# Kernel tuning notes

Hardware: AMD Instinct MI355X
Metric: run time of the kernel (lower is better)

Reference implementation:

```python
import jax, jax.numpy as jnp
from jax import lax
import numpy as np

B, T, F, H, O = 4096, 2048, 8, 32, 8


def setup_inputs() -> dict:
    key = jax.random.key(0)
    k = jax.random.split(key, 7)
    s = 1.0 / np.sqrt(H).astype(np.float32)  # torch RNN/Linear init bound
    x = jax.random.normal(k[0], (B, T, F), dtype=jnp.float32)
    W_ih = jax.random.uniform(k[1], (H, F), minval=-s, maxval=s, dtype=jnp.float32)
    W_hh = jax.random.uniform(k[2], (H, H), minval=-s, maxval=s, dtype=jnp.float32)
    b_ih = jax.random.uniform(k[3], (H,), minval=-s, maxval=s, dtype=jnp.float32)
    b_hh = jax.random.uniform(k[4], (H,), minval=-s, maxval=s, dtype=jnp.float32)
    W_out = jax.random.uniform(k[5], (O, H), minval=-s, maxval=s, dtype=jnp.float32)
    b_out = jax.random.uniform(k[6], (O,), minval=-s, maxval=s, dtype=jnp.float32)
    return {"x": x, "W_ih": W_ih, "W_hh": W_hh, "b_ih": b_ih, "b_hh": b_hh,
            "W_out": W_out, "b_out": b_out}


def reference(x, W_ih, W_hh, b_ih, b_hh, W_out, b_out):
    # Precompute input projection for all timesteps: [B, T, H]
    xp = jnp.einsum('btf,hf->bth', x, W_ih) + b_ih + b_hh
    h0 = jnp.zeros((x.shape[0], W_hh.shape[0]), dtype=x.dtype)

    def step(h, xt):  # xt: [B, H]
        h = jnp.tanh(xt + h @ W_hh.T)
        return h, None

    h_final, _ = lax.scan(step, h0, jnp.swapaxes(xp, 0, 1))  # scan over T
    # torch returns out(h) with h of shape [num_layers=1, B, H]
    y = h_final @ W_out.T + b_out  # [B, O]
    return y[None]  # [1, B, O]
```

## Files before the change

kernel.cpp:

```cpp
#include <hip/hip_runtime.h>


typedef float v2f __attribute__((ext_vector_type(2)));
typedef _Float16 h2v __attribute__((ext_vector_type(2)));

static constexpr int T_STEPS = 2048;
static constexpr int FDIM    = 8;
static constexpr int HDIM    = 32;
static constexpr int ODIM    = 8;
static constexpr int ROWS_PER_BLOCK = 8;
static constexpr int GROUP   = 4;
static constexpr int NGROUP  = T_STEPS / GROUP;
static constexpr int LSTR    = 40;

__device__ __forceinline__ float fdot2(h2v a, h2v b, float c) {
    return __builtin_amdgcn_fdot2(a, b, c, false);
}
__device__ __forceinline__ h2v bch(unsigned u) {
    return __builtin_bit_cast(h2v, u);
}

__global__ __launch_bounds__(256, 2) void rnn_scan_kernel(
    const float* __restrict__ x,
    const float* __restrict__ W_ih,
    const float* __restrict__ W_hh,
    const float* __restrict__ b_ih,
    const float* __restrict__ b_hh,
    const float* __restrict__ W_out,
    const float* __restrict__ b_out,
    float* __restrict__ out)
{
    const float K = 2.8853900817779268f;
    const int tid  = threadIdx.x;
    const int lane = tid & 63;
    const int wave = tid >> 6;
    const int g    = lane & 15;
    const int c    = (lane >> 4) & 1;
    const int sub  = lane >> 5;
    const int r    = wave * 2 + sub;
    const long long b = (long long)blockIdx.x * ROWS_PER_BLOCK + r;
    const int d0 = 2 * g, d1 = 2 * g + 1;

    __shared__ _Float16 hsh[ROWS_PER_BLOCK][LSTR];

    h2v wA[8], wB[8];
    const float* whr0 = W_hh + d0 * HDIM + 16 * c;
    const float* whr1 = W_hh + d1 * HDIM + 16 * c;
#pragma unroll
    for (int j = 0; j < 8; ++j) {
        h2v wa; wa[0] = (_Float16)(whr0[2 * j] * K); wa[1] = (_Float16)(whr0[2 * j + 1] * K);
        wA[j] = wa;
        h2v wb; wb[0] = (_Float16)(whr1[2 * j] * K); wb[1] = (_Float16)(whr1[2 * j + 1] * K);
        wB[j] = wb;
    }
    v2f wiv[4];
#pragma unroll
    for (int f = 0; f < 4; ++f) {
        v2f w; w[0] = W_ih[d0 * FDIM + 4 * c + f] * K;
               w[1] = W_ih[d1 * FDIM + 4 * c + f] * K;
        wiv[f] = w;
    }
    v2f bias2;
    bias2[0] = c ? 0.0f : (b_ih[d0] + b_hh[d0]) * K;
    bias2[1] = c ? 0.0f : (b_ih[d1] + b_hh[d1]) * K;

    hsh[r][2 * g + c] = (_Float16)0.0f;

    const float4* xq = reinterpret_cast<const float4*>(x + (size_t)b * T_STEPS * FDIM);
    const uint4* hq = reinterpret_cast<const uint4*>(
        reinterpret_cast<const char*>(&hsh[r][0]) + 32 * c);
    _Float16* hw = &hsh[r][2 * g + c];

#define LOADG(buf, gi)                                                         \
    {                                                                          \
        const int base = (gi) * (2 * GROUP) + c;                               \
        _Pragma("unroll")                                                      \
        for (int k = 0; k < GROUP; ++k) buf[k] = xq[base + 2 * k];             \
    }                                                                          \
    asm volatile("" ::: "memory");

#define STEP(xr)                                                               \
    {                                                                          \
        uint4 u0 = hq[0], u1 = hq[1];                                          \
        float c00 = 0.0f, c01 = 0.0f, c10 = 0.0f, c11 = 0.0f;                  \
        c00 = fdot2(wA[0], bch(u0.x), c00);  c10 = fdot2(wB[0], bch(u0.x), c10); \
        c01 = fdot2(wA[4], bch(u1.x), c01);  c11 = fdot2(wB[4], bch(u1.x), c11); \
        c00 = fdot2(wA[1], bch(u0.y), c00);  c10 = fdot2(wB[1], bch(u0.y), c10); \
        c01 = fdot2(wA[5], bch(u1.y), c01);  c11 = fdot2(wB[5], bch(u1.y), c11); \
        c00 = fdot2(wA[2], bch(u0.z), c00);  c10 = fdot2(wB[2], bch(u0.z), c10); \
        c01 = fdot2(wA[6], bch(u1.z), c01);  c11 = fdot2(wB[6], bch(u1.z), c11); \
        c00 = fdot2(wA[3], bch(u0.w), c00);  c10 = fdot2(wB[3], bch(u0.w), c10); \
        c01 = fdot2(wA[7], bch(u1.w), c01);  c11 = fdot2(wB[7], bch(u1.w), c11); \
        v2f a = bias2;                                                         \
        v2f t;                                                                 \
        t[0] = xr.x; t[1] = xr.x;  a = __builtin_elementwise_fma(wiv[0], t, a); \
        t[0] = xr.y; t[1] = xr.y;  a = __builtin_elementwise_fma(wiv[1], t, a); \
        t[0] = xr.z; t[1] = xr.z;  a = __builtin_elementwise_fma(wiv[2], t, a); \
        t[0] = xr.w; t[1] = xr.w;  a = __builtin_elementwise_fma(wiv[3], t, a); \
        v2f dotv; dotv[0] = c00 + c01; dotv[1] = c10 + c11;                    \
        v2f s2 = a + dotv;                                                     \
        float o0 = __int_as_float(__builtin_amdgcn_ds_swizzle(                 \
                       __float_as_int(s2[0]), 0x401f));                        \
        float o1 = __int_as_float(__builtin_amdgcn_ds_swizzle(                 \
                       __float_as_int(s2[1]), 0x401f));                        \
        float s = c ? (s2[1] + o1) : (s2[0] + o0);                             \
        float e = __builtin_amdgcn_exp2f(s);                                   \
        float rc = __builtin_amdgcn_rcpf(e + 1.0f);                            \
        *hw = (_Float16)fmaf(-2.0f, rc, 1.0f);                                 \
    }

#define STEPS(buf) STEP(buf[0]) STEP(buf[1]) STEP(buf[2]) STEP(buf[3])

    float4 bufA[GROUP], bufB[GROUP];
    LOADG(bufA, 0)

    for (int gi = 0; gi < NGROUP; gi += 2) {
        LOADG(bufB, gi + 1)
        STEPS(bufA)
        {
            const int gn = (gi + 2 < NGROUP) ? (gi + 2) : (NGROUP - 1);
            LOADG(bufA, gn)
        }
        STEPS(bufB)
    }
#undef STEPS
#undef STEP
#undef LOADG

    __syncthreads();
    if (tid < ROWS_PER_BLOCK * ODIM) {
        const int rr = tid >> 3;
        const int o  = tid & 7;
        float acc = b_out[o];
#pragma unroll
        for (int j = 0; j < HDIM; ++j)
            acc = fmaf((float)hsh[rr][j], W_out[o * HDIM + j], acc);
        out[((long long)blockIdx.x * ROWS_PER_BLOCK + rr) * ODIM + o] = acc;
    }
}

extern "C" void kernel_launch(void* const* d_in, const int* in_sizes, int n_in,
                              void* d_out, int out_size, void* d_ws, size_t ws_size,
                              hipStream_t stream) {
    const float* x     = (const float*)d_in[0];
    const float* W_ih  = (const float*)d_in[1];
    const float* W_hh  = (const float*)d_in[2];
    const float* b_ih  = (const float*)d_in[3];
    const float* b_hh  = (const float*)d_in[4];
    const float* W_out = (const float*)d_in[5];
    const float* b_out = (const float*)d_in[6];

    const int B = in_sizes[0] / (T_STEPS * FDIM);
    const int grid = B / ROWS_PER_BLOCK;

    rnn_scan_kernel<<<grid, 256, 0, stream>>>(
        x, W_ih, W_hh, b_ih, b_hh, W_out, b_out, (float*)d_out);
}
```

Measured before the change: 641.2 us.

## Keep RNN hidden state in registers via DPP permutes instead of LDS

Drops the per-step LDS store and reload of the hidden state. The state now lives in registers as a packed pair of halves, and each lane gathers the other 15 pairs through a chain of DPP row permutes, with W_hh columns reordered to match the permuted order. The cross-half reduction moves from ds_swizzle to v_permlane16_swap, and both outputs per lane are computed redundantly rather than selected. This cuts LDS latency from the serial recurrence, at the cost of eight dependent DPP moves per step and inline asm that needs exact hazard nops.

```diff
diff --git a/kernel.cpp b/kernel.cpp
--- a/kernel.cpp
+++ b/kernel.cpp
@@ -11,13 +11,30 @@
 static constexpr int ROWS_PER_BLOCK = 8;
 static constexpr int GROUP   = 4;
 static constexpr int NGROUP  = T_STEPS / GROUP;
-static constexpr int LSTR    = 40;
 
 __device__ __forceinline__ float fdot2(h2v a, h2v b, float c) {
     return __builtin_amdgcn_fdot2(a, b, c, false);
 }
 __device__ __forceinline__ h2v bch(unsigned u) {
     return __builtin_bit_cast(h2v, u);
+}
+
+template <int CTRL>
+__device__ __forceinline__ unsigned dppmov(unsigned v) {
+    return (unsigned)__builtin_amdgcn_mov_dpp((int)v, CTRL, 0xF, 0xF, true);
+}
+static constexpr int DPP_XOR1 = 0xB1;
+static constexpr int DPP_XOR2 = 0x4E;
+static constexpr int DPP_HMIR = 0x141;
+static constexpr int DPP_ROR8 = 0x128;
+
+__device__ __forceinline__ float xor16_sum(float s) {
+    float a = s, b;
+    asm("v_mov_b32 %1, %0\n\t"
+        "s_nop 1\n\t"
+        "v_permlane16_swap_b32 %0, %1"
+        : "+v"(a), "=&v"(b));
+    return a + b;
 }
 
 __global__ __launch_bounds__(256, 2) void rnn_scan_kernel(
@@ -34,23 +51,27 @@
     const int tid  = threadIdx.x;
     const int lane = tid & 63;
     const int wave = tid >> 6;
-    const int g    = lane & 15;
-    const int c    = (lane >> 4) & 1;
+    const int ll   = lane & 31;
+    const int pr   = ll & 15;
+    const int c    = ll >> 4;
     const int sub  = lane >> 5;
     const int r    = wave * 2 + sub;
     const long long b = (long long)blockIdx.x * ROWS_PER_BLOCK + r;
-    const int d0 = 2 * g, d1 = 2 * g + 1;
+    const int d0 = 2 * pr, d1 = 2 * pr + 1;
+    const int q  = (ll & 7) | (c << 3);
+    const bool fixflag = (((ll >> 3) & 1) != c);
 
-    __shared__ _Float16 hsh[ROWS_PER_BLOCK][LSTR];
+    __shared__ _Float16 hsh[ROWS_PER_BLOCK][HDIM];
 
     h2v wA[8], wB[8];
-    const float* whr0 = W_hh + d0 * HDIM + 16 * c;
-    const float* whr1 = W_hh + d1 * HDIM + 16 * c;
+    const float* whr0 = W_hh + d0 * HDIM;
+    const float* whr1 = W_hh + d1 * HDIM;
 #pragma unroll
     for (int j = 0; j < 8; ++j) {
-        h2v wa; wa[0] = (_Float16)(whr0[2 * j] * K); wa[1] = (_Float16)(whr0[2 * j + 1] * K);
+        const int kk = 2 * (q ^ j);
+        h2v wa; wa[0] = (_Float16)(whr0[kk] * K); wa[1] = (_Float16)(whr0[kk + 1] * K);
         wA[j] = wa;
-        h2v wb; wb[0] = (_Float16)(whr1[2 * j] * K); wb[1] = (_Float16)(whr1[2 * j + 1] * K);
+        h2v wb; wb[0] = (_Float16)(whr1[kk] * K); wb[1] = (_Float16)(whr1[kk + 1] * K);
         wB[j] = wb;
     }
     v2f wiv[4];
@@ -64,12 +85,9 @@
     bias2[0] = c ? 0.0f : (b_ih[d0] + b_hh[d0]) * K;
     bias2[1] = c ? 0.0f : (b_ih[d1] + b_hh[d1]) * K;
 
-    hsh[r][2 * g + c] = (_Float16)0.0f;
+    const float4* xq = reinterpret_cast<const float4*>(x + (size_t)b * T_STEPS * FDIM);
 
-    const float4* xq = reinterpret_cast<const float4*>(x + (size_t)b * T_STEPS * FDIM);
-    const uint4* hq = reinterpret_cast<const uint4*>(
-        reinterpret_cast<const char*>(&hsh[r][0]) + 32 * c);
-    _Float16* hw = &hsh[r][2 * g + c];
+    unsigned pk = 0u;
 
 #define LOADG(buf, gi)                                                         \
     {                                                                          \
@@ -81,32 +99,41 @@
 
 #define STEP(xr)                                                               \
     {                                                                          \
-        uint4 u0 = hq[0], u1 = hq[1];                                          \
+                 \
+        unsigned t8 = dppmov<DPP_ROR8>(pk);                                    \
+        unsigned g0 = fixflag ? t8 : pk;                         \
+        unsigned g1 = dppmov<DPP_XOR1>(g0);                           \
+        unsigned g2 = dppmov<DPP_XOR2>(g0);                           \
+        unsigned g3 = dppmov<DPP_XOR1>(g2);                           \
+        unsigned g4 = dppmov<DPP_HMIR>(g3);                           \
+        unsigned g5 = dppmov<DPP_HMIR>(g2);                           \
+        unsigned g6 = dppmov<DPP_HMIR>(g1);                           \
+        unsigned g7 = dppmov<DPP_HMIR>(g0);                           \
         float c00 = 0.0f, c01 = 0.0f, c10 = 0.0f, c11 = 0.0f;                  \
-        c00 = fdot2(wA[0], bch(u0.x), c00);  c10 = fdot2(wB[0], bch(u0.x), c10); \
-        c01 = fdot2(wA[4], bch(u1.x), c01);  c11 = fdot2(wB[4], bch(u1.x), c11); \
-        c00 = fdot2(wA[1], bch(u0.y), c00);  c10 = fdot2(wB[1], bch(u0.y), c10); \
-        c01 = fdot2(wA[5], bch(u1.y), c01);  c11 = fdot2(wB[5], bch(u1.y), c11); \
-        c00 = fdot2(wA[2], bch(u0.z), c00);  c10 = fdot2(wB[2], bch(u0.z), c10); \
-        c01 = fdot2(wA[6], bch(u1.z), c01);  c11 = fdot2(wB[6], bch(u1.z), c11); \
-        c00 = fdot2(wA[3], bch(u0.w), c00);  c10 = fdot2(wB[3], bch(u0.w), c10); \
-        c01 = fdot2(wA[7], bch(u1.w), c01);  c11 = fdot2(wB[7], bch(u1.w), c11); \
-        v2f a = bias2;                                                         \
+        c00 = fdot2(wA[0], bch(g0), c00);  c10 = fdot2(wB[0], bch(g0), c10);   \
+        c01 = fdot2(wA[4], bch(g4), c01);  c11 = fdot2(wB[4], bch(g4), c11);   \
+        c00 = fdot2(wA[1], bch(g1), c00);  c10 = fdot2(wB[1], bch(g1), c10);   \
+        c01 = fdot2(wA[5], bch(g5), c01);  c11 = fdot2(wB[5], bch(g5), c11);   \
+        c00 = fdot2(wA[2], bch(g2), c00);  c10 = fdot2(wB[2], bch(g2), c10);   \
+        c01 = fdot2(wA[6], bch(g6), c01);  c11 = fdot2(wB[6], bch(g6), c11);   \
+        c00 = fdot2(wA[3], bch(g3), c00);  c10 = fdot2(wB[3], bch(g3), c10);   \
+        c01 = fdot2(wA[7], bch(g7), c01);  c11 = fdot2(wB[7], bch(g7), c11);   \
+        v2f acc = bias2;                                                       \
         v2f t;                                                                 \
-        t[0] = xr.x; t[1] = xr.x;  a = __builtin_elementwise_fma(wiv[0], t, a); \
-        t[0] = xr.y; t[1] = xr.y;  a = __builtin_elementwise_fma(wiv[1], t, a); \
-        t[0] = xr.z; t[1] = xr.z;  a = __builtin_elementwise_fma(wiv[2], t, a); \
-        t[0] = xr.w; t[1] = xr.w;  a = __builtin_elementwise_fma(wiv[3], t, a); \
-        v2f dotv; dotv[0] = c00 + c01; dotv[1] = c10 + c11;                    \
-        v2f s2 = a + dotv;                                                     \
-        float o0 = __int_as_float(__builtin_amdgcn_ds_swizzle(                 \
-                       __float_as_int(s2[0]), 0x401f));                        \
-        float o1 = __int_as_float(__builtin_amdgcn_ds_swizzle(                 \
-                       __float_as_int(s2[1]), 0x401f));                        \
-        float s = c ? (s2[1] + o1) : (s2[0] + o0);                             \
-        float e = __builtin_amdgcn_exp2f(s);                                   \
-        float rc = __builtin_amdgcn_rcpf(e + 1.0f);                            \
-        *hw = (_Float16)fmaf(-2.0f, rc, 1.0f);                                 \
+        t[0] = xr.x; t[1] = xr.x;  acc = __builtin_elementwise_fma(wiv[0], t, acc); \
+        t[0] = xr.y; t[1] = xr.y;  acc = __builtin_elementwise_fma(wiv[1], t, acc); \
+        t[0] = xr.z; t[1] = xr.z;  acc = __builtin_elementwise_fma(wiv[2], t, acc); \
+        t[0] = xr.w; t[1] = xr.w;  acc = __builtin_elementwise_fma(wiv[3], t, acc); \
+        float s0 = xor16_sum(acc[0] + (c00 + c01));                            \
+        float s1 = xor16_sum(acc[1] + (c10 + c11));                            \
+        float e0 = __builtin_amdgcn_exp2f(s0);                                 \
+        float e1 = __builtin_amdgcn_exp2f(s1);                                 \
+        float r0v = __builtin_amdgcn_rcpf(e0 + 1.0f);                          \
+        float r1v = __builtin_amdgcn_rcpf(e1 + 1.0f);                          \
+        h2v hv;                                                                \
+        hv[0] = (_Float16)fmaf(-2.0f, r0v, 1.0f);                              \
+        hv[1] = (_Float16)fmaf(-2.0f, r1v, 1.0f);                              \
+        pk = __builtin_bit_cast(unsigned, hv);                                 \
     }
 
 #define STEPS(buf) STEP(buf[0]) STEP(buf[1]) STEP(buf[2]) STEP(buf[3])
@@ -127,6 +154,8 @@
 #undef STEP
 #undef LOADG
 
+    if (c == 0)
+        *reinterpret_cast<h2v*>(&hsh[r][2 * pr]) = bch(pk);
     __syncthreads();
     if (tid < ROWS_PER_BLOCK * ODIM) {
         const int rr = tid >> 3;
```

Result: slower. 817.5 us (+27.5%).

## Stream x through LDS with async global_load_lds and use permlane16 swap reduction

Applied to the files above, without the earlier changes.

Replaces per-thread register prefetch of x with asynchronous global-to-LDS loads (global_load_lds, 16 bytes per lane), double-buffered in 16-step chunks per wave and synchronized with explicit vmcnt waits. Each step then reads its x slice from LDS. The cross-half reduction switches from ds_swizzle to v_permlane16_swap via inline asm. The aim is to cut register pressure and load-latency stalls in the serial recurrence, at the cost of extra LDS traffic per step and reliance on per-wave ordering of LDS writes without barriers.

```diff
diff --git a/kernel.cpp b/kernel.cpp
--- a/kernel.cpp
+++ b/kernel.cpp
@@ -9,8 +9,9 @@
 static constexpr int HDIM    = 32;
 static constexpr int ODIM    = 8;
 static constexpr int ROWS_PER_BLOCK = 8;
-static constexpr int GROUP   = 4;
-static constexpr int NGROUP  = T_STEPS / GROUP;
+static constexpr int NWAVE   = 4;
+static constexpr int CH      = 16;
+static constexpr int NCH     = T_STEPS / CH;
 static constexpr int LSTR    = 40;
 
 __device__ __forceinline__ float fdot2(h2v a, h2v b, float c) {
@@ -18,6 +19,21 @@
 }
 __device__ __forceinline__ h2v bch(unsigned u) {
     return __builtin_bit_cast(h2v, u);
+}
+
+__device__ __forceinline__ float xor16_sum(float s) {
+    float a = s, b;
+    asm("v_mov_b32 %1, %0\n\t"
+        "s_nop 1\n\t"
+        "v_permlane16_swap_b32 %0, %1"
+        : "+v"(a), "=&v"(b));
+    return a + b;
+}
+
+__device__ __forceinline__ void gload_lds16(const void* g, void* l) {
+    __builtin_amdgcn_global_load_lds(
+        (const __attribute__((address_space(1))) void*)g,
+        (__attribute__((address_space(3))) void*)l, 16, 0, 0);
 }
 
 __global__ __launch_bounds__(256, 2) void rnn_scan_kernel(
@@ -38,10 +54,11 @@
     const int c    = (lane >> 4) & 1;
     const int sub  = lane >> 5;
     const int r    = wave * 2 + sub;
-    const long long b = (long long)blockIdx.x * ROWS_PER_BLOCK + r;
     const int d0 = 2 * g, d1 = 2 * g + 1;
 
     __shared__ _Float16 hsh[ROWS_PER_BLOCK][LSTR];
+    __shared__ alignas(16) float xA[NWAVE][CH * 16];
+    __shared__ alignas(16) float xB[NWAVE][CH * 16];
 
     h2v wA[8], wB[8];
     const float* whr0 = W_hh + d0 * HDIM + 16 * c;
@@ -66,21 +83,24 @@
 
     hsh[r][2 * g + c] = (_Float16)0.0f;
 
-    const float4* xq = reinterpret_cast<const float4*>(x + (size_t)b * T_STEPS * FDIM);
     const uint4* hq = reinterpret_cast<const uint4*>(
         reinterpret_cast<const char*>(&hsh[r][0]) + 32 * c);
     _Float16* hw = &hsh[r][2 * g + c];
 
-#define LOADG(buf, gi)                                                         \
+    const int sj = lane & 31;
+    const float* gsrc = x
+        + ((size_t)blockIdx.x * ROWS_PER_BLOCK + wave * 2 + (lane >> 5)) * ((size_t)T_STEPS * FDIM)
+        + (size_t)(sj >> 1) * FDIM + (size_t)(sj & 1) * 4;
+    float* ldstA = &xA[wave][0];
+    float* ldstB = &xB[wave][0];
+    const char* rdA = reinterpret_cast<const char*>(&xA[wave][0]) + sub * 512 + c * 16;
+    const char* rdB = reinterpret_cast<const char*>(&xB[wave][0]) + sub * 512 + c * 16;
+
+#define ISSUE(dst, chunk) gload_lds16(gsrc + (size_t)(chunk) * (CH * FDIM), dst);
+
+#define STEP(PBASE, S)                                                         \
     {                                                                          \
-        const int base = (gi) * (2 * GROUP) + c;                               \
-        _Pragma("unroll")                                                      \
-        for (int k = 0; k < GROUP; ++k) buf[k] = xq[base + 2 * k];             \
-    }                                                                          \
-    asm volatile("" ::: "memory");
-
-#define STEP(xr)                                                               \
-    {                                                                          \
+        float4 xr = *reinterpret_cast<const float4*>((PBASE) + (S) * 32);      \
         uint4 u0 = hq[0], u1 = hq[1];                                          \
         float c00 = 0.0f, c01 = 0.0f, c10 = 0.0f, c11 = 0.0f;                  \
         c00 = fdot2(wA[0], bch(u0.x), c00);  c10 = fdot2(wB[0], bch(u0.x), c10); \
@@ -99,33 +119,39 @@
         t[0] = xr.w; t[1] = xr.w;  a = __builtin_elementwise_fma(wiv[3], t, a); \
         v2f dotv; dotv[0] = c00 + c01; dotv[1] = c10 + c11;                    \
         v2f s2 = a + dotv;                                                     \
-        float o0 = __int_as_float(__builtin_amdgcn_ds_swizzle(                 \
-                       __float_as_int(s2[0]), 0x401f));                        \
-        float o1 = __int_as_float(__builtin_amdgcn_ds_swizzle(                 \
-                       __float_as_int(s2[1]), 0x401f));                        \
-        float s = c ? (s2[1] + o1) : (s2[0] + o0);                             \
-        float e = __builtin_amdgcn_exp2f(s);                                   \
-        float rc = __builtin_amdgcn_rcpf(e + 1.0f);                            \
+        float s0f = xor16_sum(s2[0]);                                          \
+        float s1f = xor16_sum(s2[1]);                                          \
+        float sv = c ? s1f : s0f;                                              \
+        float ev = __builtin_amdgcn_exp2f(sv);                                 \
+        float rc = __builtin_amdgcn_rcpf(ev + 1.0f);                           \
         *hw = (_Float16)fmaf(-2.0f, rc, 1.0f);                                 \
     }
 
-#define STEPS(buf) STEP(buf[0]) STEP(buf[1]) STEP(buf[2]) STEP(buf[3])
+#define CHUNK(PBASE)                                                           \
+    {                                                                          \
+        _Pragma("unroll")                                                      \
+        for (int st = 0; st < CH; ++st) STEP(PBASE, st)                        \
+    }
 
-    float4 bufA[GROUP], bufB[GROUP];
-    LOADG(bufA, 0)
+    ISSUE(ldstA, 0)
+    ISSUE(ldstB, 1)
 
-    for (int gi = 0; gi < NGROUP; gi += 2) {
-        LOADG(bufB, gi + 1)
-        STEPS(bufA)
-        {
-            const int gn = (gi + 2 < NGROUP) ? (gi + 2) : (NGROUP - 1);
-            LOADG(bufA, gn)
-        }
-        STEPS(bufB)
+    for (int ci = 0; ci < NCH - 2; ci += 2) {
+        asm volatile("s_waitcnt vmcnt(1)" ::: "memory");
+        CHUNK(rdA)
+        ISSUE(ldstA, ci + 2)
+        asm volatile("s_waitcnt vmcnt(1)" ::: "memory");
+        CHUNK(rdB)
+        ISSUE(ldstB, ci + 3)
     }
-#undef STEPS
+    asm volatile("s_waitcnt vmcnt(1)" ::: "memory");
+    CHUNK(rdA)
+    asm volatile("s_waitcnt vmcnt(0)" ::: "memory");
+    CHUNK(rdB)
+
+#undef CHUNK
 #undef STEP
-#undef LOADG
+#undef ISSUE
 
     __syncthreads();
     if (tid < ROWS_PER_BLOCK * ODIM) {
```

Result: slower. 666.4 us (+3.9%).
